# Performance work log

Hardware: AMD Instinct MI355X
Metric: run time of the kernel (lower is better)

Reference implementation:

```python
import jax, jax.numpy as jnp
import numpy as np

B, N = 8, 4096
NPOINT, RADIUS, NSAMPLE = 1024, 0.5, 32
IN_C = 64
MLP = [64, 64, 128]
EPS = 1e-5


def _gather(p, idx):
    # p: (B,N,C), idx: (B,...) int -> (B,...,C)
    return jax.vmap(lambda a, i: a[i])(p, idx)


def farthest_point_sample(xyz, npoint):
    b, n, _ = xyz.shape
    def step(carry, _):
        distance, farthest = carry
        centroid = _gather(xyz, farthest[:, None])              # (B,1,3)
        d = jnp.sum((xyz - centroid) ** 2, axis=-1)             # (B,N)
        distance = jnp.minimum(distance, d)
        nxt = jnp.argmax(distance, axis=-1).astype(jnp.int32)
        return (distance, nxt), farthest
    init = (jnp.full((b, n), 1e10, xyz.dtype), jnp.zeros((b,), jnp.int32))
    _, idx = jax.lax.scan(step, init, None, length=npoint)
    return idx.T                                                 # (B,npoint)


def query_ball_point(radius, nsample, xyz, new_xyz):
    b, n, _ = xyz.shape
    s = new_xyz.shape[1]
    sqr = jnp.sum((new_xyz[:, :, None, :] - xyz[:, None, :, :]) ** 2, axis=-1)  # (B,S,N)
    grp = jnp.broadcast_to(jnp.arange(n, dtype=jnp.int32), (b, s, n))
    grp = jnp.where(sqr > radius ** 2, n, grp)
    grp = jnp.sort(grp, axis=-1)[:, :, :nsample]                 # (B,S,K)
    first = grp[:, :, :1]
    return jnp.where(grp == n, first, grp)


def _sa_forward(xyz, points, params):
    fps_idx = farthest_point_sample(xyz, NPOINT)
    new_xyz = _gather(xyz, fps_idx)                              # (B,S,3)
    idx = query_ball_point(RADIUS, NSAMPLE, xyz, new_xyz)        # (B,S,K)
    grouped_xyz = _gather(xyz, idx)                              # (B,S,K,3)
    grouped_norm = grouped_xyz - new_xyz[:, :, None, :]
    grouped_pts = _gather(points, idx)                           # (B,S,K,C)
    feat = jnp.concatenate([grouped_xyz, grouped_norm, grouped_pts], axis=-1)
    for w, bias, gamma, beta in params:
        feat = jnp.einsum('bski,oi->bsko', feat, w) + bias       # 1x1 conv
        mean = feat.mean(axis=(0, 1, 2))                         # BN (train stats)
        var = feat.var(axis=(0, 1, 2))
        feat = (feat - mean) * jax.lax.rsqrt(var + EPS) * gamma + beta
        feat = jax.nn.relu(feat)
    new_points = feat.max(axis=2)                                # max over neighbors
    return new_xyz, new_points


def setup_inputs() -> dict:
    key = jax.random.key(0)
    ks = jax.random.split(key, 8)
    inp = {
        'xyz': jax.random.normal(ks[0], (B, N, 3), jnp.float32),
        'points': jax.random.normal(ks[1], (B, N, IN_C), jnp.float32),
    }
    last = IN_C + 6
    for li, out in enumerate(MLP):
        inp[f'w{li}'] = jax.random.normal(ks[2 + li], (out, last), jnp.float32) * 0.05
        inp[f'b{li}'] = jnp.zeros((out,), jnp.float32)
        inp[f'g{li}'] = jnp.ones((out,), jnp.float32)
        inp[f'be{li}'] = jnp.zeros((out,), jnp.float32)
        last = out
    return inp


def reference(xyz, points, w0, b0, g0, be0, w1, b1, g1, be1, w2, b2, g2, be2):
    params = [(w0, b0, g0, be0), (w1, b1, g1, be1), (w2, b2, g2, be2)]
    return _sa_forward(xyz, points, params)
```

## Files before the change

### kernel.cpp

```cpp
#include <hip/hip_runtime.h>

#define DI __device__ __forceinline__

#define B_ 8
#define N_ 4096
#define S_ 1024
#define K_ 32
#define M_TOT (B_ * S_ * K_)
#define NBLK 2048
#define NW 4096

typedef short bf16x8 __attribute__((ext_vector_type(8)));
typedef float f32x4 __attribute__((ext_vector_type(4)));

DI float sqdist_rn(float ax, float ay, float az, float bx, float by, float bz) {
    float dx = __fsub_rn(ax, bx);
    float dy = __fsub_rn(ay, by);
    float dz = __fsub_rn(az, bz);
    return __fadd_rn(__fadd_rn(__fmul_rn(dx, dx), __fmul_rn(dy, dy)), __fmul_rn(dz, dz));
}

DI unsigned short f2b(float f) {
    unsigned u = __float_as_uint(f);
    return (unsigned short)((u + 0x7FFFu + ((u >> 16) & 1u)) >> 16);
}
DI float b2f(unsigned short h) { return __uint_as_float(((unsigned)h) << 16); }

template <int CTRL>
DI unsigned long long dpp_u64(unsigned long long v) {
    unsigned lo = (unsigned)__builtin_amdgcn_update_dpp(
        0, (int)(unsigned)v, CTRL, 0xF, 0xF, true);
    unsigned hi = (unsigned)__builtin_amdgcn_update_dpp(
        0, (int)(unsigned)(v >> 32), CTRL, 0xF, 0xF, true);
    return ((unsigned long long)hi << 32) | lo;
}
DI unsigned long long umax64(unsigned long long a, unsigned long long b) {
    return a > b ? a : b;
}

struct FpsSh { float4 pts[N_]; unsigned long long part[2][8]; };
struct WrkSh { float feat[128 * 76]; float wl[64 * 76]; int idxl[128]; };
union MegaSh { FpsSh f; WrkSh w; char pad[84 * 1024]; };

DI void fps_role(const float* __restrict__ xyz, float* __restrict__ new_xyz,
                 unsigned* __restrict__ cnt, MegaSh& sh) {
    const int b = blockIdx.x;
    const int t = threadIdx.x;
    const float* X = xyz + (size_t)b * (N_ * 3);
    float px[8], py[8], pz[8], dd[8];
#pragma unroll
    for (int j = 0; j < 8; ++j) {
        int p = t + 512 * j;
        float x = X[p * 3 + 0], y = X[p * 3 + 1], z = X[p * 3 + 2];
        px[j] = x; py[j] = y; pz[j] = z; dd[j] = 1e10f;
        sh.f.pts[p] = make_float4(x, y, z, 0.0f);
    }
    if (t == 0) {
        new_xyz[(size_t)b * (S_ * 3) + 0] = px[0];
        new_xyz[(size_t)b * (S_ * 3) + 1] = py[0];
        new_xyz[(size_t)b * (S_ * 3) + 2] = pz[0];
    }
    __syncthreads();
    float4 cent = sh.f.pts[0];
    for (int i = 1; i < S_; ++i) {
        unsigned long long k0[8];
#pragma unroll
        for (int j = 0; j < 8; ++j) {
            float d = sqdist_rn(px[j], py[j], pz[j], cent.x, cent.y, cent.z);
            dd[j] = fminf(dd[j], d);
            k0[j] = ((unsigned long long)__float_as_uint(dd[j]) << 32) |
                    (unsigned long long)(~(unsigned)(t + 512 * j));
        }
        k0[0] = umax64(k0[0], k0[1]);
        k0[2] = umax64(k0[2], k0[3]);
        k0[4] = umax64(k0[4], k0[5]);
        k0[6] = umax64(k0[6], k0[7]);
        k0[0] = umax64(k0[0], k0[2]);
        k0[4] = umax64(k0[4], k0[6]);
        unsigned long long key = umax64(k0[0], k0[4]);
        key = umax64(key, dpp_u64<0x111>(key));
        key = umax64(key, dpp_u64<0x112>(key));
        key = umax64(key, dpp_u64<0x114>(key));
        key = umax64(key, dpp_u64<0x118>(key));
        key = umax64(key, dpp_u64<0x142>(key));
        key = umax64(key, dpp_u64<0x143>(key));
        if ((t & 63) == 63) sh.f.part[i & 1][t >> 6] = key;
        __syncthreads();
        ulonglong2 q0 = *(const ulonglong2*)&sh.f.part[i & 1][0];
        ulonglong2 q1 = *(const ulonglong2*)&sh.f.part[i & 1][2];
        ulonglong2 q2 = *(const ulonglong2*)&sh.f.part[i & 1][4];
        ulonglong2 q3 = *(const ulonglong2*)&sh.f.part[i & 1][6];
        unsigned long long ka = umax64(umax64(q0.x, q0.y), umax64(q1.x, q1.y));
        unsigned long long kb = umax64(umax64(q2.x, q2.y), umax64(q3.x, q3.y));
        unsigned long long k = umax64(ka, kb);
        unsigned gidx = ~(unsigned)(k & 0xFFFFFFFFull);
        cent = sh.f.pts[gidx];
        if (t == 0) {
            size_t o3 = ((size_t)b * S_ + i) * 3;
            new_xyz[o3 + 0] = cent.x;
            new_xyz[o3 + 1] = cent.y;
            new_xyz[o3 + 2] = cent.z;
            if ((i & 31) == 31) {
                __threadfence();
                __hip_atomic_store(&cnt[b], (unsigned)(i + 1),
                                   __ATOMIC_RELEASE, __HIP_MEMORY_SCOPE_AGENT);
            }
        }
    }
}

DI void gemm512(const float* __restrict__ feat, const float* __restrict__ wl,
                const float* __restrict__ bias, unsigned short* __restrict__ yout,
                float* __restrict__ ps, float* __restrict__ pq, int tile, int tid) {
    const int tr = tid & 15;
    const int tc = tid >> 4;
    const int r0 = tile * 128;
    float acc[8][2];
#pragma unroll
    for (int rr = 0; rr < 8; ++rr) { acc[rr][0] = 0.f; acc[rr][1] = 0.f; }
#pragma unroll 2
    for (int sl = 0; sl < 18; ++sl) {
        float4 xv[8], wv[2];
#pragma unroll
        for (int rr = 0; rr < 8; ++rr)
            xv[rr] = *(const float4*)&feat[(tr + 16 * rr) * 76 + 4 * sl];
#pragma unroll
        for (int cc = 0; cc < 2; ++cc)
            wv[cc] = *(const float4*)&wl[(tc + 32 * cc) * 76 + 4 * sl];
#pragma unroll
        for (int rr = 0; rr < 8; ++rr)
#pragma unroll
            for (int cc = 0; cc < 2; ++cc)
                acc[rr][cc] = fmaf(xv[rr].x, wv[cc].x,
                               fmaf(xv[rr].y, wv[cc].y,
                                fmaf(xv[rr].z, wv[cc].z,
                                 fmaf(xv[rr].w, wv[cc].w, acc[rr][cc]))));
    }
#pragma unroll
    for (int cc = 0; cc < 2; ++cc) {
        const int och = tc + 32 * cc;
        const float bv = bias[och];
        float s1 = 0.f, s2 = 0.f;
#pragma unroll
        for (int rr = 0; rr < 8; ++rr) {
            float y = acc[rr][cc] + bv;
            yout[(size_t)(r0 + tr + 16 * rr) * 64 + och] = f2b(y);
            s1 += y;
            s2 = fmaf(y, y, s2);
        }
#pragma unroll
        for (int m = 1; m < 16; m <<= 1) {
            s1 += __shfl_xor(s1, m);
            s2 += __shfl_xor(s2, m);
        }
        if ((tid & 15) == 0) {
            ps[och * NBLK + tile] = s1;
            pq[och * NBLK + tile] = s2;
        }
    }
}

DI void worker_role(const float* __restrict__ xyz, const float* __restrict__ points,
                    const float* __restrict__ new_xyz, const float* __restrict__ W0,
                    const float* __restrict__ bias0, unsigned short* __restrict__ yout,
                    float* __restrict__ ps, float* __restrict__ pq,
                    const unsigned* __restrict__ cnt, MegaSh& sh, int nWrk) {
    const int t = threadIdx.x;
    for (int g = (int)blockIdx.x - 8; g < 2048; g += nWrk) {
        const int q = g >> 3;
        const int b = g & 7;
        const int s0 = q * 4;
        const int tile = b * 256 + q;
        if (t == 0) {
            while (__hip_atomic_load(&cnt[b], __ATOMIC_ACQUIRE,
                                     __HIP_MEMORY_SCOPE_AGENT) < (unsigned)(s0 + 4))
                __builtin_amdgcn_s_sleep(32);
        }
        __syncthreads();
        const int w = t >> 6, lane = t & 63;
        if (w < 4) {
            const int c = b * 1024 + s0 + w;
            const float* X = xyz + (size_t)b * (N_ * 3);
            const float cx = new_xyz[c * 3 + 0];
            const float cy = new_xyz[c * 3 + 1];
            const float cz = new_xyz[c * 3 + 2];
            int* out = &sh.w.idxl[w * K_];
            int taken = 0, first = -1;
            for (int ch = 0; ch < 64; ++ch) {
                int p = ch * 64 + lane;
                float d = sqdist_rn(X[p * 3 + 0], X[p * 3 + 1], X[p * 3 + 2], cx, cy, cz);
                bool ok = (d <= 0.25f);
                unsigned long long m = __ballot(ok);
                if (first < 0 && m) first = ch * 64 + (__ffsll((unsigned long long)m) - 1);
                int pos = taken + (int)__popcll(m & ((1ull << lane) - 1ull));
                if (ok && pos < K_) out[pos] = p;
                taken += (int)__popcll(m);
                if (taken >= K_) break;
            }
            int filled = taken < K_ ? taken : K_;
            if (lane >= filled && lane < K_) out[lane] = first;
        }
        __syncthreads();
        for (int jj = t; jj < 64 * 70; jj += 512) {
            int o = jj / 70;
            int i2 = jj - o * 70;
            int mch = (i2 < 6) ? i2 : (i2 + 2);
            sh.w.wl[o * 76 + mch] = W0[jj];
        }
        if (t < 128) sh.w.wl[(t >> 1) * 76 + 6 + (t & 1)] = 0.0f;
        {
            const int row = t >> 2, h = t & 3;
            const int k = row & 31, cloc = row >> 5;
            const int pi = sh.w.idxl[cloc * 32 + k];
            const float* P = points + ((size_t)b * N_ + pi) * 64 + h * 16;
            float* fr = &sh.w.feat[row * 76];
#pragma unroll
            for (int qq = 0; qq < 4; ++qq)
                *(float4*)(fr + 8 + h * 16 + 4 * qq) = *(const float4*)(P + 4 * qq);
            if (h == 0) {
                size_t pb = ((size_t)b * N_ + pi) * 3;
                float x = xyz[pb + 0], y = xyz[pb + 1], z = xyz[pb + 2];
                const float* C = new_xyz + ((size_t)b * S_ + s0 + cloc) * 3;
                fr[0] = x; fr[1] = y; fr[2] = z;
                fr[3] = x - C[0]; fr[4] = y - C[1]; fr[5] = z - C[2];
                fr[6] = 0.0f; fr[7] = 0.0f;
            }
        }
        __syncthreads();
        gemm512(sh.w.feat, sh.w.wl, bias0, yout, ps, pq, tile, t);
        __syncthreads();
    }
}

__global__ __launch_bounds__(512) void mega_kernel(
    const float* __restrict__ xyz, const float* __restrict__ points,
    float* __restrict__ new_xyz, const float* __restrict__ w0,
    const float* __restrict__ b0, unsigned short* __restrict__ y1,
    float* __restrict__ ps, float* __restrict__ pq,
    unsigned* __restrict__ cnt, int nWrk) {
    __shared__ MegaSh sh;
    if (blockIdx.x < 8)
        fps_role(xyz, new_xyz, cnt, sh);
    else
        worker_role(xyz, points, new_xyz, w0, b0, y1, ps, pq, cnt, sh, nWrk);
}

template <int OC, bool LAST>
__global__ __launch_bounds__(256) void layerM_kernel(
    const unsigned short* __restrict__ yin,
    const float* __restrict__ scale, const float* __restrict__ shift,
    const float* __restrict__ W, const float* __restrict__ bias,
    unsigned short* __restrict__ yout,
    float* __restrict__ ps, float* __restrict__ pq,
    float* __restrict__ maxb, float* __restrict__ minb) {
    const int tid = threadIdx.x;
    const int blk = blockIdx.x;
    const int r0 = blk * 256;
    __shared__ unsigned short featA[256 * 64];
    __shared__ unsigned short wlT[OC * 64];
    __shared__ float ssc[64], ssh[64];
    if (tid < 64) { ssc[tid] = scale[tid]; ssh[tid] = shift[tid]; }
#pragma unroll
    for (int it = 0; it < OC / 16; ++it) {
        int q = it * 256 + tid;
        int och = q >> 4;
        int qq = q & 15;
        float4 wv = *(const float4*)&W[q * 4];
        uint2 pk;
        pk.x = (unsigned)f2b(wv.x) | ((unsigned)f2b(wv.y) << 16);
        pk.y = (unsigned)f2b(wv.z) | ((unsigned)f2b(wv.w) << 16);
        int idx = och * 64 + (((qq * 8) ^ ((och & 7) << 4)) >> 1);
        *(uint2*)&wlT[idx] = pk;
    }
    __syncthreads();
#pragma unroll
    for (int it = 0; it < 8; ++it) {
        int f = it * 256 + tid;
        int row = f >> 3, g = f & 7;
        uint4 u = *(const uint4*)&yin[(size_t)(r0 + row) * 64 + g * 8];
        int c = g * 8;
        float f0 = fmaxf(fmaf(__uint_as_float(u.x << 16),         ssc[c + 0], ssh[c + 0]), 0.f);
        float f1 = fmaxf(fmaf(__uint_as_float(u.x & 0xFFFF0000u), ssc[c + 1], ssh[c + 1]), 0.f);
        float f2 = fmaxf(fmaf(__uint_as_float(u.y << 16),         ssc[c + 2], ssh[c + 2]), 0.f);
        float f3 = fmaxf(fmaf(__uint_as_float(u.y & 0xFFFF0000u), ssc[c + 3], ssh[c + 3]), 0.f);
        float f4 = fmaxf(fmaf(__uint_as_float(u.z << 16),         ssc[c + 4], ssh[c + 4]), 0.f);
        float f5 = fmaxf(fmaf(__uint_as_float(u.z & 0xFFFF0000u), ssc[c + 5], ssh[c + 5]), 0.f);
        float f6 = fmaxf(fmaf(__uint_as_float(u.w << 16),         ssc[c + 6], ssh[c + 6]), 0.f);
        float f7 = fmaxf(fmaf(__uint_as_float(u.w & 0xFFFF0000u), ssc[c + 7], ssh[c + 7]), 0.f);
        uint4 pk;
        pk.x = (unsigned)f2b(f0) | ((unsigned)f2b(f1) << 16);
        pk.y = (unsigned)f2b(f2) | ((unsigned)f2b(f3) << 16);
        pk.z = (unsigned)f2b(f4) | ((unsigned)f2b(f5) << 16);
        pk.w = (unsigned)f2b(f6) | ((unsigned)f2b(f7) << 16);
        int idx = row * 64 + (((g * 16) ^ ((row & 7) << 4)) >> 1);
        *(uint4*)&featA[idx] = pk;
    }
    __syncthreads();
    const int w = tid >> 6, l = tid & 63;
    const int lr = l & 15, lg = l >> 4;
    const int wrow0 = w * 64;
    f32x4 acc[4][OC / 16];
#pragma unroll
    for (int mf = 0; mf < 4; ++mf)
#pragma unroll
        for (int nf = 0; nf < OC / 16; ++nf)
#pragma unroll
            for (int r = 0; r < 4; ++r) acc[mf][nf][r] = 0.0f;
#pragma unroll
    for (int kc = 0; kc < 2; ++kc) {
        const int kb = kc * 64 + lg * 16;
        bf16x8 bfr[OC / 16];
#pragma unroll
        for (int nf = 0; nf < OC / 16; ++nf) {
            int och = nf * 16 + lr;
            bfr[nf] = *(const bf16x8*)&wlT[och * 64 + ((kb ^ ((och & 7) << 4)) >> 1)];
        }
#pragma unroll
        for (int mf = 0; mf < 4; ++mf) {
            int row = wrow0 + mf * 16 + lr;
            bf16x8 af = *(const bf16x8*)&featA[row * 64 + ((kb ^ ((row & 7) << 4)) >> 1)];
#pragma unroll
            for (int nf = 0; nf < OC / 16; ++nf)
                acc[mf][nf] = __builtin_amdgcn_mfma_f32_16x16x32_bf16(
                    af, bfr[nf], acc[mf][nf], 0, 0, 0);
        }
    }
    const int gwave = blk * 4 + w;
#pragma unroll
    for (int nf = 0; nf < OC / 16; ++nf) {
        const int och = nf * 16 + lr;
        const float bv = bias[och];
        float s1 = 0.f, s2 = 0.f;
        float mx0 = -1e30f, mn0 = 1e30f, mx1 = -1e30f, mn1 = 1e30f;
#pragma unroll
    for (int mf = 0; mf < 4; ++mf) {
#pragma unroll
            for (int r = 0; r < 4; ++r) {
                float y = acc[mf][nf][r] + bv;
                s1 += y;
                s2 = fmaf(y, y, s2);
                if (LAST) {
                    if (mf < 2) { mx0 = fmaxf(mx0, y); mn0 = fminf(mn0, y); }
                    else        { mx1 = fmaxf(mx1, y); mn1 = fminf(mn1, y); }
                } else {
                    int gr = r0 + wrow0 + mf * 16 + lg * 4 + r;
                    yout[(size_t)gr * OC + och] = f2b(y);
                }
            }
        }
        s1 += __shfl_xor(s1, 16); s1 += __shfl_xor(s1, 32);
        s2 += __shfl_xor(s2, 16); s2 += __shfl_xor(s2, 32);
        if (LAST) {
            mx0 = fmaxf(mx0, __shfl_xor(mx0, 16)); mx0 = fmaxf(mx0, __shfl_xor(mx0, 32));
            mn0 = fminf(mn0, __shfl_xor(mn0, 16)); mn0 = fminf(mn0, __shfl_xor(mn0, 32));
            mx1 = fmaxf(mx1, __shfl_xor(mx1, 16)); mx1 = fmaxf(mx1, __shfl_xor(mx1, 32));
            mn1 = fminf(mn1, __shfl_xor(mn1, 16)); mn1 = fminf(mn1, __shfl_xor(mn1, 32));
        }
        if (l < 16) {
            ps[och * NW + gwave] = s1;
            pq[och * NW + gwave] = s2;
            if (LAST) {
                int grp0 = blk * 8 + w * 2;
                maxb[(size_t)grp0 * OC + och] = mx0;
                minb[(size_t)grp0 * OC + och] = mn0;
                maxb[(size_t)(grp0 + 1) * OC + och] = mx1;
                minb[(size_t)(grp0 + 1) * OC + och] = mn1;
            }
        }
    }
}

template <int NPART>
__global__ __launch_bounds__(256) void bn_reduce_kernel(
    const float* __restrict__ ps, const float* __restrict__ pq,
    const float* __restrict__ gamma, const float* __restrict__ beta,
    float* __restrict__ scale, float* __restrict__ shift) {
    const int o = blockIdx.x, t = threadIdx.x;
    float s1 = 0.f, s2 = 0.f;
    for (int i = t; i < NPART; i += 256) {
        s1 += ps[o * NPART + i];
        s2 += pq[o * NPART + i];
    }
#pragma unroll
    for (int m = 32; m >= 1; m >>= 1) { s1 += __shfl_xor(s1, m); s2 += __shfl_xor(s2, m); }
    __shared__ float a1[4], a2[4];
    if ((t & 63) == 0) { a1[t >> 6] = s1; a2[t >> 6] = s2; }
    __syncthreads();
    if (t == 0) {
        float S1 = a1[0] + a1[1] + a1[2] + a1[3];
        float S2 = a2[0] + a2[1] + a2[2] + a2[3];
        const float inv = 1.0f / (float)M_TOT;
        float mean = S1 * inv;
        float var = S2 * inv - mean * mean;
        if (var < 0.f) var = 0.f;
        float rstd = 1.0f / sqrtf(var + 1e-5f);
        float sc = rstd * gamma[o];
        scale[o] = sc;
        shift[o] = beta[o] - mean * sc;
    }
}

__global__ __launch_bounds__(256) void pool2_kernel(
    const float* __restrict__ maxb, const float* __restrict__ minb,
    const float* __restrict__ scale, const float* __restrict__ shift,
    float* __restrict__ outp) {
    int idx = blockIdx.x * 256 + threadIdx.x;
    int och = idx & 127;
    float sc = scale[och], sh = shift[och];
    float a = fmaf(maxb[idx], sc, sh);
    float b = fmaf(minb[idx], sc, sh);
    outp[idx] = fmaxf(fmaxf(a, b), 0.0f);
}

extern "C" void kernel_launch(void* const* d_in, const int* in_sizes, int n_in,
                              void* d_out, int out_size, void* d_ws, size_t ws_size,
                              hipStream_t stream) {
    const float* xyz    = (const float*)d_in[0];
    const float* points = (const float*)d_in[1];
    const float* w0  = (const float*)d_in[2];
    const float* b0  = (const float*)d_in[3];
    const float* g0  = (const float*)d_in[4];
    const float* be0 = (const float*)d_in[5];
    const float* w1  = (const float*)d_in[6];
    const float* b1  = (const float*)d_in[7];
    const float* g1  = (const float*)d_in[8];
    const float* be1 = (const float*)d_in[9];
    const float* w2  = (const float*)d_in[10];
    const float* b2  = (const float*)d_in[11];
    const float* g2  = (const float*)d_in[12];
    const float* be2 = (const float*)d_in[13];

    float* out = (float*)d_out;
    char* ws = (char*)d_ws;
    unsigned* cnt = (unsigned*)ws;
    float* ps  = (float*)(ws + (1 << 20));
    float* pq  = (float*)(ws + (3 << 20));
    float* st  = (float*)(ws + (5 << 20));
    float *sc0 = st,        *sh0 = st + 128;
    float *sc1 = st + 256,  *sh1 = st + 384;
    float *sc2 = st + 512,  *sh2 = st + 640;
    float* maxb = (float*)(ws + (6 << 20));
    float* minb = (float*)(ws + (10 << 20));
    unsigned short* y1 = (unsigned short*)(ws + (14 << 20));
    unsigned short* y2 = (unsigned short*)(ws + (46 << 20));

    int blocksPerCU = 0;
    hipOccupancyMaxActiveBlocksPerMultiprocessor(&blocksPerCU, mega_kernel, 512, 0);
    if (blocksPerCU < 1) blocksPerCU = 1;
    int grid = blocksPerCU * 256;
    if (grid > 2056) grid = 2056;
    int nWrk = grid - 8;

    hipMemsetAsync(cnt, 0, 8 * sizeof(unsigned), stream);

    void* args[] = {(void*)&xyz, (void*)&points, (void*)&out, (void*)&w0, (void*)&b0,
                    (void*)&y1, (void*)&ps, (void*)&pq, (void*)&cnt, (void*)&nWrk};
    hipLaunchCooperativeKernel(mega_kernel, dim3(grid), dim3(512), args, 0, stream);

    bn_reduce_kernel<NBLK><<<64, 256, 0, stream>>>(ps, pq, g0, be0, sc0, sh0);
    layerM_kernel<64, false><<<M_TOT / 256, 256, 0, stream>>>(
        y1, sc0, sh0, w1, b1, y2, ps, pq, nullptr, nullptr);
    bn_reduce_kernel<NW><<<64, 256, 0, stream>>>(ps, pq, g1, be1, sc1, sh1);
    layerM_kernel<128, true><<<M_TOT / 256, 256, 0, stream>>>(
        y2, sc1, sh1, w2, b2, nullptr, ps, pq, maxb, minb);
    bn_reduce_kernel<NW><<<128, 256, 0, stream>>>(ps, pq, g2, be2, sc2, sh2);
    pool2_kernel<<<4096, 256, 0, stream>>>(maxb, minb, sc2, sh2, out + 24576);
}
```

Measured before the change: 856.5 us.

## Switch MLP intermediates to fp16 with packed BN-ReLU and tighten FPS argmax

Intermediate activations and weights move from bf16 to fp16. BN+ReLU is now applied with packed half2 math, and the MFMA uses the f16 variant. FPS does its per-thread argmax on floats before building a single 64-bit key, and reduces the 8 wave partials with DPP instead of each thread reading all of them. The per-batch progress counters are spread onto separate cache lines and the spin-wait sleep is lengthened. fp16 has less range than bf16 and computing BN in half precision may cost accuracy.

```diff
diff --git a/kernel.cpp b/kernel.cpp
--- a/kernel.cpp
+++ b/kernel.cpp
@@ -9,9 +9,12 @@
 #define M_TOT (B_ * S_ * K_)
 #define NBLK 2048
 #define NW 4096
-
-typedef short bf16x8 __attribute__((ext_vector_type(8)));
+#define CSTRIDE 32
+
 typedef float f32x4 __attribute__((ext_vector_type(4)));
+typedef _Float16 f16x8v __attribute__((ext_vector_type(8)));
+typedef _Float16 f16x2v __attribute__((ext_vector_type(2)));
+typedef __fp16 fp16x2b __attribute__((ext_vector_type(2)));
 
 DI float sqdist_rn(float ax, float ay, float az, float bx, float by, float bz) {
     float dx = __fsub_rn(ax, bx);
@@ -20,11 +23,23 @@
     return __fadd_rn(__fadd_rn(__fmul_rn(dx, dx), __fmul_rn(dy, dy)), __fmul_rn(dz, dz));
 }
 
-DI unsigned short f2b(float f) {
-    unsigned u = __float_as_uint(f);
-    return (unsigned short)((u + 0x7FFFu + ((u >> 16) & 1u)) >> 16);
-}
-DI float b2f(unsigned short h) { return __uint_as_float(((unsigned)h) << 16); }
+DI unsigned pkrtz(float a, float b) {
+    fp16x2b h = __builtin_amdgcn_cvt_pkrtz(a, b);
+    unsigned u; __builtin_memcpy(&u, &h, 4); return u;
+}
+DI unsigned short f2h(float f) {
+    _Float16 h = (_Float16)f; unsigned short s; __builtin_memcpy(&s, &h, 2); return s;
+}
+DI unsigned bnrelu2(unsigned y, unsigned sc, unsigned sh) {
+    f16x2v hy, hsc, hsh;
+    __builtin_memcpy(&hy, &y, 4);
+    __builtin_memcpy(&hsc, &sc, 4);
+    __builtin_memcpy(&hsh, &sh, 4);
+    f16x2v r = hy * hsc + hsh;
+    f16x2v z = {(_Float16)0, (_Float16)0};
+    r = __builtin_elementwise_max(r, z);
+    unsigned u; __builtin_memcpy(&u, &r, 4); return u;
+}
 
 template <int CTRL>
 DI unsigned long long dpp_u64(unsigned long long v) {
@@ -46,6 +61,7 @@
                  unsigned* __restrict__ cnt, MegaSh& sh) {
     const int b = blockIdx.x;
     const int t = threadIdx.x;
+    const int lane = t & 63;
     const float* X = xyz + (size_t)b * (N_ * 3);
     float px[8], py[8], pz[8], dd[8];
 #pragma unroll
@@ -63,37 +79,36 @@
     __syncthreads();
     float4 cent = sh.f.pts[0];
     for (int i = 1; i < S_; ++i) {
-        unsigned long long k0[8];
 #pragma unroll
         for (int j = 0; j < 8; ++j) {
             float d = sqdist_rn(px[j], py[j], pz[j], cent.x, cent.y, cent.z);
             dd[j] = fminf(dd[j], d);
-            k0[j] = ((unsigned long long)__float_as_uint(dd[j]) << 32) |
-                    (unsigned long long)(~(unsigned)(t + 512 * j));
-        }
-        k0[0] = umax64(k0[0], k0[1]);
-        k0[2] = umax64(k0[2], k0[3]);
-        k0[4] = umax64(k0[4], k0[5]);
-        k0[6] = umax64(k0[6], k0[7]);
-        k0[0] = umax64(k0[0], k0[2]);
-        k0[4] = umax64(k0[4], k0[6]);
-        unsigned long long key = umax64(k0[0], k0[4]);
+        }
+        float m01 = dd[1] > dd[0] ? dd[1] : dd[0];  unsigned j01 = dd[1] > dd[0] ? 1u : 0u;
+        float m23 = dd[3] > dd[2] ? dd[3] : dd[2];  unsigned j23 = dd[3] > dd[2] ? 3u : 2u;
+        float m45 = dd[5] > dd[4] ? dd[5] : dd[4];  unsigned j45 = dd[5] > dd[4] ? 5u : 4u;
+        float m67 = dd[7] > dd[6] ? dd[7] : dd[6];  unsigned j67 = dd[7] > dd[6] ? 7u : 6u;
+        float m03 = m23 > m01 ? m23 : m01;          unsigned j03 = m23 > m01 ? j23 : j01;
+        float m47 = m67 > m45 ? m67 : m45;          unsigned j47 = m67 > m45 ? j67 : j45;
+        float mb  = m47 > m03 ? m47 : m03;          unsigned jb  = m47 > m03 ? j47 : j03;
+        unsigned bp = (unsigned)t + (jb << 9);
+        unsigned long long key =
+            ((unsigned long long)__float_as_uint(mb) << 32) |
+            (unsigned long long)(~bp);
         key = umax64(key, dpp_u64<0x111>(key));
         key = umax64(key, dpp_u64<0x112>(key));
         key = umax64(key, dpp_u64<0x114>(key));
         key = umax64(key, dpp_u64<0x118>(key));
         key = umax64(key, dpp_u64<0x142>(key));
         key = umax64(key, dpp_u64<0x143>(key));
-        if ((t & 63) == 63) sh.f.part[i & 1][t >> 6] = key;
+        if (lane == 63) sh.f.part[i & 1][t >> 6] = key;
         __syncthreads();
-        ulonglong2 q0 = *(const ulonglong2*)&sh.f.part[i & 1][0];
-        ulonglong2 q1 = *(const ulonglong2*)&sh.f.part[i & 1][2];
-        ulonglong2 q2 = *(const ulonglong2*)&sh.f.part[i & 1][4];
-        ulonglong2 q3 = *(const ulonglong2*)&sh.f.part[i & 1][6];
-        unsigned long long ka = umax64(umax64(q0.x, q0.y), umax64(q1.x, q1.y));
-        unsigned long long kb = umax64(umax64(q2.x, q2.y), umax64(q3.x, q3.y));
-        unsigned long long k = umax64(ka, kb);
-        unsigned gidx = ~(unsigned)(k & 0xFFFFFFFFull);
+        unsigned long long pk = 0;
+        if (lane < 8) pk = sh.f.part[i & 1][lane];
+        pk = umax64(pk, dpp_u64<0x111>(pk));
+        pk = umax64(pk, dpp_u64<0x112>(pk));
+        pk = umax64(pk, dpp_u64<0x114>(pk));
+        unsigned gidx = ~(unsigned)__builtin_amdgcn_readlane((int)(unsigned)pk, 7);
         cent = sh.f.pts[gidx];
         if (t == 0) {
             size_t o3 = ((size_t)b * S_ + i) * 3;
@@ -102,7 +117,7 @@
             new_xyz[o3 + 2] = cent.z;
             if ((i & 31) == 31) {
                 __threadfence();
-                __hip_atomic_store(&cnt[b], (unsigned)(i + 1),
+                __hip_atomic_store(&cnt[b * CSTRIDE], (unsigned)(i + 1),
                                    __ATOMIC_RELEASE, __HIP_MEMORY_SCOPE_AGENT);
             }
         }
@@ -144,7 +159,7 @@
 #pragma unroll
         for (int rr = 0; rr < 8; ++rr) {
             float y = acc[rr][cc] + bv;
-            yout[(size_t)(r0 + tr + 16 * rr) * 64 + och] = f2b(y);
+            yout[(size_t)(r0 + tr + 16 * rr) * 64 + och] = f2h(y);
             s1 += y;
             s2 = fmaf(y, y, s2);
         }
@@ -172,9 +187,9 @@
         const int s0 = q * 4;
         const int tile = b * 256 + q;
         if (t == 0) {
-            while (__hip_atomic_load(&cnt[b], __ATOMIC_ACQUIRE,
+            while (__hip_atomic_load(&cnt[b * CSTRIDE], __ATOMIC_ACQUIRE,
                                      __HIP_MEMORY_SCOPE_AGENT) < (unsigned)(s0 + 4))
-                __builtin_amdgcn_s_sleep(32);
+                __builtin_amdgcn_s_sleep(64);
         }
         __syncthreads();
         const int w = t >> 6, lane = t & 63;
@@ -258,8 +273,11 @@
     const int r0 = blk * 256;
     __shared__ unsigned short featA[256 * 64];
     __shared__ unsigned short wlT[OC * 64];
-    __shared__ float ssc[64], ssh[64];
-    if (tid < 64) { ssc[tid] = scale[tid]; ssh[tid] = shift[tid]; }
+    __shared__ unsigned ssc2[32], ssh2[32];
+    if (tid < 32) {
+        ssc2[tid] = pkrtz(scale[2 * tid], scale[2 * tid + 1]);
+        ssh2[tid] = pkrtz(shift[2 * tid], shift[2 * tid + 1]);
+    }
 #pragma unroll
     for (int it = 0; it < OC / 16; ++it) {
         int q = it * 256 + tid;
@@ -267,8 +285,8 @@
         int qq = q & 15;
         float4 wv = *(const float4*)&W[q * 4];
         uint2 pk;
-        pk.x = (unsigned)f2b(wv.x) | ((unsigned)f2b(wv.y) << 16);
-        pk.y = (unsigned)f2b(wv.z) | ((unsigned)f2b(wv.w) << 16);
+        pk.x = pkrtz(wv.x, wv.y);
+        pk.y = pkrtz(wv.z, wv.w);
         int idx = och * 64 + (((qq * 8) ^ ((och & 7) << 4)) >> 1);
         *(uint2*)&wlT[idx] = pk;
     }
@@ -278,20 +296,12 @@
         int f = it * 256 + tid;
         int row = f >> 3, g = f & 7;
         uint4 u = *(const uint4*)&yin[(size_t)(r0 + row) * 64 + g * 8];
-        int c = g * 8;
-        float f0 = fmaxf(fmaf(__uint_as_float(u.x << 16),         ssc[c + 0], ssh[c + 0]), 0.f);
-        float f1 = fmaxf(fmaf(__uint_as_float(u.x & 0xFFFF0000u), ssc[c + 1], ssh[c + 1]), 0.f);
-        float f2 = fmaxf(fmaf(__uint_as_float(u.y << 16),         ssc[c + 2], ssh[c + 2]), 0.f);
-        float f3 = fmaxf(fmaf(__uint_as_float(u.y & 0xFFFF0000u), ssc[c + 3], ssh[c + 3]), 0.f);
-        float f4 = fmaxf(fmaf(__uint_as_float(u.z << 16),         ssc[c + 4], ssh[c + 4]), 0.f);
-        float f5 = fmaxf(fmaf(__uint_as_float(u.z & 0xFFFF0000u), ssc[c + 5], ssh[c + 5]), 0.f);
-        float f6 = fmaxf(fmaf(__uint_as_float(u.w << 16),         ssc[c + 6], ssh[c + 6]), 0.f);
-        float f7 = fmaxf(fmaf(__uint_as_float(u.w & 0xFFFF0000u), ssc[c + 7], ssh[c + 7]), 0.f);
+        int c2 = g * 4;
         uint4 pk;
-        pk.x = (unsigned)f2b(f0) | ((unsigned)f2b(f1) << 16);
-        pk.y = (unsigned)f2b(f2) | ((unsigned)f2b(f3) << 16);
-        pk.z = (unsigned)f2b(f4) | ((unsigned)f2b(f5) << 16);
-        pk.w = (unsigned)f2b(f6) | ((unsigned)f2b(f7) << 16);
+        pk.x = bnrelu2(u.x, ssc2[c2 + 0], ssh2[c2 + 0]);
+        pk.y = bnrelu2(u.y, ssc2[c2 + 1], ssh2[c2 + 1]);
+        pk.z = bnrelu2(u.z, ssc2[c2 + 2], ssh2[c2 + 2]);
+        pk.w = bnrelu2(u.w, ssc2[c2 + 3], ssh2[c2 + 3]);
         int idx = row * 64 + (((g * 16) ^ ((row & 7) << 4)) >> 1);
         *(uint4*)&featA[idx] = pk;
     }
@@ -309,19 +319,19 @@
 #pragma unroll
     for (int kc = 0; kc < 2; ++kc) {
         const int kb = kc * 64 + lg * 16;
-        bf16x8 bfr[OC / 16];
+        f16x8v bfr[OC / 16];
 #pragma unroll
         for (int nf = 0; nf < OC / 16; ++nf) {
             int och = nf * 16 + lr;
-            bfr[nf] = *(const bf16x8*)&wlT[och * 64 + ((kb ^ ((och & 7) << 4)) >> 1)];
+            bfr[nf] = *(const f16x8v*)&wlT[och * 64 + ((kb ^ ((och & 7) << 4)) >> 1)];
         }
 #pragma unroll
         for (int mf = 0; mf < 4; ++mf) {
             int row = wrow0 + mf * 16 + lr;
-            bf16x8 af = *(const bf16x8*)&featA[row * 64 + ((kb ^ ((row & 7) << 4)) >> 1)];
+            f16x8v af = *(const f16x8v*)&featA[row * 64 + ((kb ^ ((row & 7) << 4)) >> 1)];
 #pragma unroll
             for (int nf = 0; nf < OC / 16; ++nf)
-                acc[mf][nf] = __builtin_amdgcn_mfma_f32_16x16x32_bf16(
+                acc[mf][nf] = __builtin_amdgcn_mfma_f32_16x16x32_f16(
                     af, bfr[nf], acc[mf][nf], 0, 0, 0);
         }
     }
@@ -333,7 +343,7 @@
         float s1 = 0.f, s2 = 0.f;
         float mx0 = -1e30f, mn0 = 1e30f, mx1 = -1e30f, mn1 = 1e30f;
 #pragma unroll
-    for (int mf = 0; mf < 4; ++mf) {
+        for (int mf = 0; mf < 4; ++mf) {
 #pragma unroll
             for (int r = 0; r < 4; ++r) {
                 float y = acc[mf][nf][r] + bv;
@@ -344,7 +354,7 @@
                     else        { mx1 = fmaxf(mx1, y); mn1 = fminf(mn1, y); }
                 } else {
                     int gr = r0 + wrow0 + mf * 16 + lg * 4 + r;
-                    yout[(size_t)gr * OC + och] = f2b(y);
+                    yout[(size_t)gr * OC + och] = f2h(y);
                 }
             }
         }
@@ -445,17 +455,17 @@
     unsigned short* y2 = (unsigned short*)(ws + (46 << 20));
 
     int blocksPerCU = 0;
-    hipOccupancyMaxActiveBlocksPerMultiprocessor(&blocksPerCU, mega_kernel, 512, 0);
+    (void)hipOccupancyMaxActiveBlocksPerMultiprocessor(&blocksPerCU, mega_kernel, 512, 0);
     if (blocksPerCU < 1) blocksPerCU = 1;
     int grid = blocksPerCU * 256;
     if (grid > 2056) grid = 2056;
     int nWrk = grid - 8;
 
-    hipMemsetAsync(cnt, 0, 8 * sizeof(unsigned), stream);
+    (void)hipMemsetAsync(cnt, 0, 8 * CSTRIDE * sizeof(unsigned), stream);
 
     void* args[] = {(void*)&xyz, (void*)&points, (void*)&out, (void*)&w0, (void*)&b0,
                     (void*)&y1, (void*)&ps, (void*)&pq, (void*)&cnt, (void*)&nWrk};
-    hipLaunchCooperativeKernel(mega_kernel, dim3(grid), dim3(512), args, 0, stream);
+    (void)hipLaunchCooperativeKernel(mega_kernel, dim3(grid), dim3(512), args, 0, stream);
 
     bn_reduce_kernel<NBLK><<<64, 256, 0, stream>>>(ps, pq, g0, be0, sc0, sh0);
     layerM_kernel<64, false><<<M_TOT / 256, 256, 0, stream>>>(
```

Result: no change. 870.3 us (+1.6%).
